# Kernel tuning notes

Hardware: AMD Instinct MI355X
Metric: run time of the kernel (lower is better)

Reference implementation:

```python
import jax, jax.numpy as jnp
import numpy as np

NUM_EMBEDDINGS = 1024
EMBEDDING_DIM = 256
COMMITMENT_COST = 0.25


def setup_inputs() -> dict:
    key = jax.random.key(0)
    k1, k2 = jax.random.split(key)
    z = jax.random.normal(k1, (64, 32, 32, EMBEDDING_DIM), dtype=jnp.float32)
    # torch init: uniform(-1/num_embeddings, 1/num_embeddings)
    codebook = jax.random.uniform(
        k2, (NUM_EMBEDDINGS, EMBEDDING_DIM), dtype=jnp.float32,
        minval=-1.0 / NUM_EMBEDDINGS, maxval=1.0 / NUM_EMBEDDINGS)
    return {"z": z, "codebook": codebook}


def reference(z, codebook):
    sg = jax.lax.stop_gradient
    D = codebook.shape[1]
    flat_z = z.reshape(-1, D)  # [N, D]
    # squared L2 distances: ||z||^2 + ||e||^2 - 2 z.e  -> [N, K]
    distances = (jnp.sum(flat_z * flat_z, axis=1, keepdims=True)
                 + jnp.sum(codebook * codebook, axis=1)
                 - 2.0 * jnp.matmul(flat_z, codebook.T))
    indices = jnp.argmin(distances, axis=1)  # [N]
    quantized = codebook[indices].reshape(z.shape)
    e_latent_loss = jnp.mean((quantized - sg(z)) ** 2)
    q_latent_loss = jnp.mean((z - sg(quantized)) ** 2)
    vq_loss = e_latent_loss + COMMITMENT_COST * q_latent_loss
    # straight-through estimator
    quantized_st = z + sg(quantized - z)
    return quantized_st, vq_loss, indices.reshape(z.shape[:-1])
```

## Files before the change

kernel.cpp:

```cpp
#include <hip/hip_runtime.h>

#pragma clang fp contract(off)


#define NROWS   65536
#define DDIM    256
#define KCODES  1024
#define QSIZE   (NROWS * DDIM)
#define LOSS_OFF QSIZE
#define IDX_OFF (QSIZE + 1)
#define MARGIN  3.0e-4f
#define RBATCH  16

typedef __bf16 bf16x8 __attribute__((ext_vector_type(8)));
typedef float f32x4 __attribute__((ext_vector_type(4)));
typedef unsigned int u32;
typedef unsigned long long u64;
typedef unsigned short u16;
typedef unsigned char u8;

#define GLOAD_LDS16(gsrc, ldst) \
    __builtin_amdgcn_global_load_lds( \
        (const __attribute__((address_space(1))) u32*)(gsrc), \
        (__attribute__((address_space(3))) u32*)(ldst), 16, 0, 0)

__device__ __forceinline__ u32 omap(float s) {
    u32 u = __float_as_uint(s);
    return (u & 0x80000000u) ? ~u : (u | 0x80000000u);
}
__device__ __forceinline__ u64 pack_key(float s, u32 j) {
    return ((u64)omap(s) << 32) | j;
}

__device__ __forceinline__ float pw128_sq(const float* __restrict__ x) {
    float r[8];
    #pragma unroll
    for (int j = 0; j < 8; ++j) r[j] = x[j] * x[j];
    for (int i = 8; i < 128; i += 8)
        #pragma unroll
        for (int j = 0; j < 8; ++j) r[j] += x[i + j] * x[i + j];
    return ((r[0] + r[1]) + (r[2] + r[3])) + ((r[4] + r[5]) + (r[6] + r[7]));
}

__global__ __launch_bounds__(256) void vq_pack_cb(
    const float* __restrict__ E, u16* __restrict__ ebh,
    float4* __restrict__ etp,
    float* __restrict__ ee, float* __restrict__ sum) {
    int j = blockIdx.x * 256 + threadIdx.x;
    if (j == 0) *sum = 0.0f;
    if (j >= KCODES) return;
    const float* row = E + (size_t)j * DDIM;
    const float4* row4 = (const float4*)row;
    #pragma unroll
    for (int d4 = 0; d4 < DDIM / 4; ++d4) etp[d4 * KCODES + j] = row4[d4];
    #pragma unroll
    for (int ks = 0; ks < 32; ++ks) {
        bf16x8 h8;
        #pragma unroll
        for (int e = 0; e < 8; ++e) h8[e] = (__bf16)row[ks * 8 + e];
        *(bf16x8*)(ebh + ((size_t)ks * KCODES + j) * 8) = h8;
    }
    ee[j] = pw128_sq(row) + pw128_sq(row + 128);
}

__device__ __forceinline__ void stage_chunk32(
    const u16* __restrict__ ebh, int codebase, char* buf, int t) {
    #pragma unroll
    for (int i = 0; i < 4; ++i) {
        int p = t + 256 * i;
        int ks = p >> 5, c = p & 31;
        GLOAD_LDS16(ebh + ((size_t)ks * KCODES + codebase + c) * 8, buf + p * 16);
    }
}

__global__ __launch_bounds__(256, 4) void vq_gemm(
    const float* __restrict__ Z,
    const u16* __restrict__ ebh,
    const float* __restrict__ ee,
    float* __restrict__ s1c, float* __restrict__ s2c, float* __restrict__ i1c,
    float* __restrict__ sum) {
    __shared__ __align__(16) char bs[3][16384];
    const int t = threadIdx.x, w = t >> 6, l = t & 63;
    const int lr = l & 15, lg = l >> 4;
    const int rowtile = blockIdx.x >> 1, half = blockIdx.x & 1;
    const int rowbase = rowtile * 128;
    const int codebase = half * 512;

    bf16x8 aH[2][8];
    float ss = 0.0f;
    #pragma unroll
    for (int rf = 0; rf < 2; ++rf) {
        const float* zr = Z + (size_t)(rowbase + w * 32 + rf * 16 + lr) * DDIM;
        #pragma unroll
        for (int s = 0; s < 8; ++s) {
            const float4* src = (const float4*)(zr + (s * 4 + lg) * 8);
            float4 v0 = src[0], v1 = src[1];
            bf16x8 h8;
            h8[0] = (__bf16)v0.x; h8[1] = (__bf16)v0.y;
            h8[2] = (__bf16)v0.z; h8[3] = (__bf16)v0.w;
            h8[4] = (__bf16)v1.x; h8[5] = (__bf16)v1.y;
            h8[6] = (__bf16)v1.z; h8[7] = (__bf16)v1.w;
            aH[rf][s] = h8;
            ss += v0.x * v0.x + v0.y * v0.y + v0.z * v0.z + v0.w * v0.w
                + v1.x * v1.x + v1.y * v1.y + v1.z * v1.z + v1.w * v1.w;
        }
    }
    if (half == 0) {
        #pragma unroll
        for (int off = 1; off < 64; off <<= 1) ss += __shfl_xor(ss, off);
        if (l == 0) atomicAdd(sum, ss);
    }

    float s1[2][4], s2[2][4]; int i1[2][4];
    #pragma unroll
    for (int rf = 0; rf < 2; ++rf)
        #pragma unroll
        for (int r = 0; r < 4; ++r) { s1[rf][r] = 1e30f; s2[rf][r] = 1e30f; i1[rf][r] = 0x7FFFFFFF; }

    stage_chunk32(ebh, codebase, bs[0], t);
    stage_chunk32(ebh, codebase + 32, bs[1], t);
    for (int ch = 0; ch < 16; ++ch) {
        if (ch < 15) { asm volatile("s_waitcnt vmcnt(4)" ::: "memory"); }
        else         { asm volatile("s_waitcnt vmcnt(0)" ::: "memory"); }
        __builtin_amdgcn_sched_barrier(0);
        __builtin_amdgcn_s_barrier();
        if (ch + 2 < 16) stage_chunk32(ebh, codebase + (ch + 2) * 32, bs[(ch + 2) % 3], t);
        const char* buf = bs[ch % 3];
        const int chbase = codebase + ch * 32;

        f32x4 acc[2][2];
        #pragma unroll
        for (int rf = 0; rf < 2; ++rf)
            #pragma unroll
            for (int cf = 0; cf < 2; ++cf) acc[rf][cf] = 0.0f;

        #pragma unroll
        for (int s = 0; s < 8; ++s) {
            #pragma unroll
            for (int cf = 0; cf < 2; ++cf) {
                int off = (((s * 4 + lg) * 32 + cf * 16 + lr) * 16);
                bf16x8 bh = *(const bf16x8*)(buf + off);
                #pragma unroll
                for (int rf = 0; rf < 2; ++rf)
                    acc[rf][cf] = __builtin_amdgcn_mfma_f32_16x16x32_bf16(aH[rf][s], bh, acc[rf][cf], 0, 0, 0);
            }
        }
        #pragma unroll
        for (int cf = 0; cf < 2; ++cf) {
            int code = chbase + cf * 16 + lr;
            float e2c = ee[code];
            #pragma unroll
            for (int rf = 0; rf < 2; ++rf)
                #pragma unroll
                for (int r = 0; r < 4; ++r) {
                    float v = __fmaf_rn(-2.0f, acc[rf][cf][r], e2c);
                    float so = s1[rf][r];
                    s2[rf][r] = fminf(fmaxf(so, v), s2[rf][r]);
                    bool lt = v < so;
                    s1[rf][r] = lt ? v : so;
                    i1[rf][r] = lt ? code : i1[rf][r];
                }
        }
    }
    #pragma unroll
    for (int off = 1; off < 16; off <<= 1) {
        #pragma unroll
        for (int rf = 0; rf < 2; ++rf)
            #pragma unroll
            for (int r = 0; r < 4; ++r) {
                float os1 = __shfl_xor(s1[rf][r], off);
                float os2 = __shfl_xor(s2[rf][r], off);
                int   oi  = __shfl_xor(i1[rf][r], off);
                float ns2 = fminf(fmaxf(s1[rf][r], os1), fminf(s2[rf][r], os2));
                bool take = (os1 < s1[rf][r]) || (os1 == s1[rf][r] && oi < i1[rf][r]);
                s1[rf][r] = take ? os1 : s1[rf][r];
                i1[rf][r] = take ? oi : i1[rf][r];
                s2[rf][r] = ns2;
            }
    }
    if (lr == 0) {
        #pragma unroll
        for (int rf = 0; rf < 2; ++rf)
            #pragma unroll
            for (int r = 0; r < 4; ++r) {
                size_t idx = (size_t)half * NROWS + rowbase + w * 32 + rf * 16 + lg * 4 + r;
                s1c[idx] = s1[rf][r];
                s2c[idx] = s2[rf][r];
                i1c[idx] = (float)i1[rf][r];
            }
    }
}

__global__ __launch_bounds__(256) void vq_combine(
    const float* __restrict__ s1c, const float* __restrict__ s2c,
    const float* __restrict__ i1c,
    float* out, float* __restrict__ sum, u8* __restrict__ flags) {
    const int r = blockIdx.x * 256 + threadIdx.x;
    float s1a = s1c[r], s1b = s1c[NROWS + r];
    float s2a = s2c[r], s2b = s2c[NROWS + r];
    int   ia  = (int)i1c[r], ib = (int)i1c[NROWS + r];
    bool tb = s1b < s1a;
    float s1 = tb ? s1b : s1a;
    int   i1 = tb ? ib : ia;
    float s2 = tb ? fminf(s2b, s1a) : fminf(s2a, s1b);
    out[(size_t)IDX_OFF + r] = (float)i1;
    flags[r] = (s2 <= s1 + MARGIN) ? 1 : 0;
    #pragma unroll
    for (int off = 1; off < 64; off <<= 1) s1 += __shfl_xor(s1, off);
    if ((threadIdx.x & 63) == 0) atomicAdd(sum, s1);
}

__global__ __launch_bounds__(256) void vq_rescueq(
    const float* __restrict__ Z, const float4* __restrict__ etp,
    const float* __restrict__ ee, const float* __restrict__ E,
    const u8* __restrict__ flags, const float* __restrict__ sum,
    float* out) {
    __shared__ float zrow[RBATCH][DDIM];
    __shared__ float zacc[RBATCH][16];
    __shared__ float z2s[RBATCH];
    __shared__ u64 rmin[RBATCH];
    __shared__ int qidx[128];
    __shared__ int fl[128];
    __shared__ int nfl;
    const int t = threadIdx.x;
    const int b = blockIdx.x;
    const int rowbase = b * 128;

    if (b == 0 && t == 0) out[LOSS_OFF] = 1.25f * (*sum) / (float)QSIZE;
    if (t == 0) nfl = 0;
    __syncthreads();
    if (t < 128) {
        int code = (int)out[(size_t)IDX_OFF + rowbase + t];
        qidx[t] = code;
        if (flags[rowbase + t]) { int s = atomicAdd(&nfl, 1); fl[s] = t; }
    }
    __syncthreads();
    const int n = nfl;

    for (int start = 0; start < n; start += RBATCH) {
        int nb = n - start; if (nb > RBATCH) nb = RBATCH;
        if (t < RBATCH) rmin[t] = ~0ULL;
        __syncthreads();
        #pragma unroll
        for (int i = 0; i < RBATCH * (DDIM / 4) / 256; ++i) {
            int p = t + 256 * i;
            int r = p >> 6, c4 = p & 63;
            if (r < nb) ((float4*)zrow[r])[c4] =
                ((const float4*)(Z + (size_t)(rowbase + fl[start + r]) * DDIM))[c4];
        }
        __syncthreads();
        if (t < RBATCH * 8) {
            int r = t >> 3, j = t & 7;
            const float* zr = zrow[r];
            float a0 = zr[j] * zr[j], a1 = zr[128 + j] * zr[128 + j];
            for (int i = 8; i < 128; i += 8) {
                a0 += zr[i + j] * zr[i + j];
                a1 += zr[128 + i + j] * zr[128 + i + j];
            }
            zacc[r][j] = a0; zacc[r][8 + j] = a1;
        }
        __syncthreads();
        if (t < RBATCH) {
            const float* a = zacc[t];
            float c0 = ((a[0] + a[1]) + (a[2] + a[3])) + ((a[4] + a[5]) + (a[6] + a[7]));
            float c1 = ((a[8] + a[9]) + (a[10] + a[11])) + ((a[12] + a[13]) + (a[14] + a[15]));
            z2s[t] = c0 + c1;
        }
        __syncthreads();
        float acc[4][RBATCH];
        #pragma unroll
        for (int c = 0; c < 4; ++c)
            #pragma unroll
            for (int r = 0; r < RBATCH; ++r) acc[c][r] = 0.0f;
        for (int d4 = 0; d4 < DDIM / 4; ++d4) {
            float4 ev[4];
            #pragma unroll
            for (int c = 0; c < 4; ++c)
                ev[c] = etp[(size_t)d4 * KCODES + t + c * 256];
            #pragma unroll
            for (int r = 0; r < RBATCH; ++r) {
                float4 zv = ((const float4*)zrow[r])[d4];
                #pragma unroll
                for (int c = 0; c < 4; ++c) {
                    float a = acc[c][r];
                    a = __fmaf_rn(zv.x, ev[c].x, a); a = __fmaf_rn(zv.y, ev[c].y, a);
                    a = __fmaf_rn(zv.z, ev[c].z, a); a = __fmaf_rn(zv.w, ev[c].w, a);
                    acc[c][r] = a;
                }
            }
        }
        float e2c[4];
        #pragma unroll
        for (int c = 0; c < 4; ++c) e2c[c] = ee[t + c * 256];
        #pragma unroll
        for (int r = 0; r < RBATCH; ++r) {
            float zr2 = z2s[r];
            u64 best = ~0ULL;
            #pragma unroll
            for (int c = 0; c < 4; ++c) {
                float d = (zr2 + e2c[c]) - 2.0f * acc[c][r];
                u64 k = pack_key(d, (u32)(t + c * 256));
                if (k < best) best = k;
            }
            #pragma unroll
            for (int off = 1; off < 64; off <<= 1) {
                u64 o = __shfl_xor(best, off);
                if (o < best) best = o;
            }
            if ((t & 63) == 0) atomicMin(&rmin[r], best);
        }
        __syncthreads();
        if (t < nb) {
            int lrow = fl[start + t];
            int code = (int)(u32)(rmin[t] & 0xFFFFFFFFu);
            out[(size_t)IDX_OFF + rowbase + lrow] = (float)code;
            qidx[lrow] = code;
        }
        __syncthreads();
    }

    float4* outq = (float4*)out;
    #pragma unroll
    for (int k = 0; k < 32; ++k) {
        int p = t + 256 * k;
        int r = p >> 6, c4 = p & 63;
        int code = qidx[r];
        outq[(size_t)rowbase * 64 + p] = ((const float4*)(E + (size_t)code * DDIM))[c4];
    }
}

extern "C" void kernel_launch(void* const* d_in, const int* in_sizes, int n_in,
                              void* d_out, int out_size, void* d_ws, size_t ws_size,
                              hipStream_t stream) {
    const float* Z; const float* E;
    if (in_sizes[0] == QSIZE) { Z = (const float*)d_in[0]; E = (const float*)d_in[1]; }
    else                      { Z = (const float*)d_in[1]; E = (const float*)d_in[0]; }
    float* out = (float*)d_out;
    char* ws = (char*)d_ws;

    float*  sum   = (float*)ws;
    float*  ee    = (float*)(ws + 1024);
    u16*    ebh   = (u16*)(ws + 8192);
    u8*     flags = (u8*)(ws + 532480);
    float4* etp   = (float4*)(ws + 598016);

    float* s1c = out;
    float* s2c = out + 2 * NROWS;
    float* i1c = out + 4 * NROWS;

    vq_pack_cb<<<4, 256, 0, stream>>>(E, ebh, etp, ee, sum);
    vq_gemm<<<NROWS / 128 * 2, 256, 0, stream>>>(Z, ebh, ee, s1c, s2c, i1c, sum);
    vq_combine<<<NROWS / 256, 256, 0, stream>>>(s1c, s2c, i1c, out, sum, flags);
    vq_rescueq<<<NROWS / 128, 256, 0, stream>>>(Z, etp, ee, E, flags, sum, out);
}
```

Baseline: 198.8 us.

## Fuse combine pass into rescue kernel and finalize loss with last-block counter

```diff
diff --git a/kernel.cpp b/kernel.cpp
--- a/kernel.cpp
+++ b/kernel.cpp
@@ -10,14 +10,13 @@
 #define LOSS_OFF QSIZE
 #define IDX_OFF (QSIZE + 1)
 #define MARGIN  3.0e-4f
-#define RBATCH  16
+#define RB      8
 
 typedef __bf16 bf16x8 __attribute__((ext_vector_type(8)));
 typedef float f32x4 __attribute__((ext_vector_type(4)));
 typedef unsigned int u32;
 typedef unsigned long long u64;
 typedef unsigned short u16;
-typedef unsigned char u8;
 
 #define GLOAD_LDS16(gsrc, ldst) \
     __builtin_amdgcn_global_load_lds( \
@@ -45,9 +44,9 @@
 __global__ __launch_bounds__(256) void vq_pack_cb(
     const float* __restrict__ E, u16* __restrict__ ebh,
     float4* __restrict__ etp,
-    float* __restrict__ ee, float* __restrict__ sum) {
+    float* __restrict__ ee, float* __restrict__ sum, int* __restrict__ done) {
     int j = blockIdx.x * 256 + threadIdx.x;
-    if (j == 0) *sum = 0.0f;
+    if (j == 0) { *sum = 0.0f; *done = 0; }
     if (j >= KCODES) return;
     const float* row = E + (size_t)j * DDIM;
     const float4* row4 = (const float4*)row;
@@ -77,8 +76,7 @@
     const float* __restrict__ Z,
     const u16* __restrict__ ebh,
     const float* __restrict__ ee,
-    float* __restrict__ s1c, float* __restrict__ s2c, float* __restrict__ i1c,
-    float* __restrict__ sum) {
+    float* __restrict__ out, float* __restrict__ sum) {
     __shared__ __align__(16) char bs[3][16384];
     const int t = threadIdx.x, w = t >> 6, l = t & 63;
     const int lr = l & 15, lg = l >> 4;
@@ -183,42 +181,23 @@
         for (int rf = 0; rf < 2; ++rf)
             #pragma unroll
             for (int r = 0; r < 4; ++r) {
-                size_t idx = (size_t)half * NROWS + rowbase + w * 32 + rf * 16 + lg * 4 + r;
-                s1c[idx] = s1[rf][r];
-                s2c[idx] = s2[rf][r];
-                i1c[idx] = (float)i1[rf][r];
-            }
-    }
-}
-
-__global__ __launch_bounds__(256) void vq_combine(
-    const float* __restrict__ s1c, const float* __restrict__ s2c,
-    const float* __restrict__ i1c,
-    float* out, float* __restrict__ sum, u8* __restrict__ flags) {
-    const int r = blockIdx.x * 256 + threadIdx.x;
-    float s1a = s1c[r], s1b = s1c[NROWS + r];
-    float s2a = s2c[r], s2b = s2c[NROWS + r];
-    int   ia  = (int)i1c[r], ib = (int)i1c[NROWS + r];
-    bool tb = s1b < s1a;
-    float s1 = tb ? s1b : s1a;
-    int   i1 = tb ? ib : ia;
-    float s2 = tb ? fminf(s2b, s1a) : fminf(s2a, s1b);
-    out[(size_t)IDX_OFF + r] = (float)i1;
-    flags[r] = (s2 <= s1 + MARGIN) ? 1 : 0;
-    #pragma unroll
-    for (int off = 1; off < 64; off <<= 1) s1 += __shfl_xor(s1, off);
-    if ((threadIdx.x & 63) == 0) atomicAdd(sum, s1);
+                size_t row = (size_t)rowbase + w * 32 + rf * 16 + lg * 4 + r;
+                float* c = out + row * DDIM + half * 3;
+                c[0] = s1[rf][r];
+                c[1] = s2[rf][r];
+                c[2] = (float)i1[rf][r];
+            }
+    }
 }
 
 __global__ __launch_bounds__(256) void vq_rescueq(
     const float* __restrict__ Z, const float4* __restrict__ etp,
     const float* __restrict__ ee, const float* __restrict__ E,
-    const u8* __restrict__ flags, const float* __restrict__ sum,
-    float* out) {
-    __shared__ float zrow[RBATCH][DDIM];
-    __shared__ float zacc[RBATCH][16];
-    __shared__ float z2s[RBATCH];
-    __shared__ u64 rmin[RBATCH];
+    float* __restrict__ sum, int* __restrict__ done, float* __restrict__ out) {
+    __shared__ float zrow[RB][DDIM];
+    __shared__ float zacc[RB][16];
+    __shared__ float z2s[RB];
+    __shared__ u64 rmin[RB];
     __shared__ int qidx[128];
     __shared__ int fl[128];
     __shared__ int nfl;
@@ -226,30 +205,39 @@
     const int b = blockIdx.x;
     const int rowbase = b * 128;
 
-    if (b == 0 && t == 0) out[LOSS_OFF] = 1.25f * (*sum) / (float)QSIZE;
     if (t == 0) nfl = 0;
     __syncthreads();
+
     if (t < 128) {
-        int code = (int)out[(size_t)IDX_OFF + rowbase + t];
-        qidx[t] = code;
-        if (flags[rowbase + t]) { int s = atomicAdd(&nfl, 1); fl[s] = t; }
+        const float* c = out + (size_t)(rowbase + t) * DDIM;
+        float s1a = c[0], s2a = c[1]; int ia = (int)c[2];
+        float s1b = c[3], s2b = c[4]; int ib = (int)c[5];
+        bool tb = s1b < s1a;
+        float s1 = tb ? s1b : s1a;
+        int   i1 = tb ? ib : ia;
+        float s2 = tb ? fminf(s2b, s1a) : fminf(s2a, s1b);
+        qidx[t] = i1;
+        if (s2 <= s1 + MARGIN) { int s = atomicAdd(&nfl, 1); fl[s] = t; }
+        #pragma unroll
+        for (int off = 1; off < 64; off <<= 1) s1 += __shfl_xor(s1, off);
+        if ((t & 63) == 0) atomicAdd(sum, s1);
     }
     __syncthreads();
     const int n = nfl;
 
-    for (int start = 0; start < n; start += RBATCH) {
-        int nb = n - start; if (nb > RBATCH) nb = RBATCH;
-        if (t < RBATCH) rmin[t] = ~0ULL;
-        __syncthreads();
-        #pragma unroll
-        for (int i = 0; i < RBATCH * (DDIM / 4) / 256; ++i) {
+    for (int start = 0; start < n; start += RB) {
+        int nb = n - start; if (nb > RB) nb = RB;
+        if (t < RB) rmin[t] = ~0ULL;
+        __syncthreads();
+        #pragma unroll
+        for (int i = 0; i < RB * (DDIM / 4) / 256; ++i) {
             int p = t + 256 * i;
             int r = p >> 6, c4 = p & 63;
             if (r < nb) ((float4*)zrow[r])[c4] =
                 ((const float4*)(Z + (size_t)(rowbase + fl[start + r]) * DDIM))[c4];
         }
         __syncthreads();
-        if (t < RBATCH * 8) {
+        if (t < RB * 8) {
             int r = t >> 3, j = t & 7;
             const float* zr = zrow[r];
             float a0 = zr[j] * zr[j], a1 = zr[128 + j] * zr[128 + j];
@@ -260,25 +248,25 @@
             zacc[r][j] = a0; zacc[r][8 + j] = a1;
         }
         __syncthreads();
-        if (t < RBATCH) {
+        if (t < RB) {
             const float* a = zacc[t];
             float c0 = ((a[0] + a[1]) + (a[2] + a[3])) + ((a[4] + a[5]) + (a[6] + a[7]));
             float c1 = ((a[8] + a[9]) + (a[10] + a[11])) + ((a[12] + a[13]) + (a[14] + a[15]));
             z2s[t] = c0 + c1;
         }
         __syncthreads();
-        float acc[4][RBATCH];
+        float acc[4][RB];
         #pragma unroll
         for (int c = 0; c < 4; ++c)
             #pragma unroll
-            for (int r = 0; r < RBATCH; ++r) acc[c][r] = 0.0f;
+            for (int r = 0; r < RB; ++r) acc[c][r] = 0.0f;
         for (int d4 = 0; d4 < DDIM / 4; ++d4) {
             float4 ev[4];
             #pragma unroll
             for (int c = 0; c < 4; ++c)
                 ev[c] = etp[(size_t)d4 * KCODES + t + c * 256];
             #pragma unroll
-            for (int r = 0; r < RBATCH; ++r) {
+            for (int r = 0; r < RB; ++r) {
                 float4 zv = ((const float4*)zrow[r])[d4];
                 #pragma unroll
                 for (int c = 0; c < 4; ++c) {
@@ -293,7 +281,7 @@
         #pragma unroll
         for (int c = 0; c < 4; ++c) e2c[c] = ee[t + c * 256];
         #pragma unroll
-        for (int r = 0; r < RBATCH; ++r) {
+        for (int r = 0; r < RB; ++r) {
             float zr2 = z2s[r];
             u64 best = ~0ULL;
             #pragma unroll
@@ -310,15 +298,11 @@
             if ((t & 63) == 0) atomicMin(&rmin[r], best);
         }
         __syncthreads();
-        if (t < nb) {
-            int lrow = fl[start + t];
-            int code = (int)(u32)(rmin[t] & 0xFFFFFFFFu);
-            out[(size_t)IDX_OFF + rowbase + lrow] = (float)code;
-            qidx[lrow] = code;
-        }
-        __syncthreads();
-    }
-
+        if (t < nb) qidx[fl[start + t]] = (int)(u32)(rmin[t] & 0xFFFFFFFFu);
+        __syncthreads();
+    }
+
+    if (t < 128) out[(size_t)IDX_OFF + rowbase + t] = (float)qidx[t];
     float4* outq = (float4*)out;
     #pragma unroll
     for (int k = 0; k < 32; ++k) {
@@ -326,6 +310,18 @@
         int r = p >> 6, c4 = p & 63;
         int code = qidx[r];
         outq[(size_t)rowbase * 64 + p] = ((const float4*)(E + (size_t)code * DDIM))[c4];
+    }
+
+    __threadfence();
+    __syncthreads();
+    if (t == 0) {
+        int pos = __hip_atomic_fetch_add(done, 1, __ATOMIC_ACQ_REL,
+                                         __HIP_MEMORY_SCOPE_AGENT);
+        if (pos == (int)gridDim.x - 1) {
+            float s = __hip_atomic_load(sum, __ATOMIC_RELAXED,
+                                        __HIP_MEMORY_SCOPE_AGENT);
+            out[LOSS_OFF] = 1.25f * s / (float)QSIZE;
+        }
     }
 }
 
@@ -338,18 +334,13 @@
     float* out = (float*)d_out;
     char* ws = (char*)d_ws;
 
-    float*  sum   = (float*)ws;
-    float*  ee    = (float*)(ws + 1024);
-    u16*    ebh   = (u16*)(ws + 8192);
-    u8*     flags = (u8*)(ws + 532480);
-    float4* etp   = (float4*)(ws + 598016);
-
-    float* s1c = out;
-    float* s2c = out + 2 * NROWS;
-    float* i1c = out + 4 * NROWS;
-
-    vq_pack_cb<<<4, 256, 0, stream>>>(E, ebh, etp, ee, sum);
-    vq_gemm<<<NROWS / 128 * 2, 256, 0, stream>>>(Z, ebh, ee, s1c, s2c, i1c, sum);
-    vq_combine<<<NROWS / 256, 256, 0, stream>>>(s1c, s2c, i1c, out, sum, flags);
-    vq_rescueq<<<NROWS / 128, 256, 0, stream>>>(Z, etp, ee, E, flags, sum, out);
-}
+    float*  sum  = (float*)ws;
+    int*    done = (int*)(ws + 8);
+    float*  ee   = (float*)(ws + 1024);
+    u16*    ebh  = (u16*)(ws + 8192);
+    float4* etp  = (float4*)(ws + 532480);
+
+    vq_pack_cb<<<4, 256, 0, stream>>>(E, ebh, etp, ee, sum, done);
+    vq_gemm<<<NROWS / 128 * 2, 256, 0, stream>>>(Z, ebh, ee, out, sum);
+    vq_rescueq<<<NROWS / 128, 256, 0, stream>>>(Z, etp, ee, E, sum, done, out);
+}
```

Result: slower. 281.3 us (+41.5%).
